# Optimization experiments

Hardware: AMD Instinct MI355X
Metric: run time of the kernel (lower is better)

## Reference

```python
import jax, jax.numpy as jnp
import numpy as np

N_NODES = 50000
N_EDGES = 800000
IN_CH = 256
HID_CH = 128


def setup_inputs() -> dict:
    key = jax.random.key(0)
    k1, k2, k3, k4, k5 = jax.random.split(key, 5)
    x = jax.random.normal(k1, (N_NODES, IN_CH), dtype=jnp.float32)
    edge_index = jax.random.randint(k2, (2, N_EDGES), 0, N_NODES, dtype=jnp.int64)
    edge_weight = jax.random.uniform(k3, (N_EDGES,), dtype=jnp.float32)
    W = jax.random.normal(k4, (IN_CH, HID_CH), dtype=jnp.float32) * (1.0 / np.sqrt(IN_CH))
    b = jnp.zeros((HID_CH,), dtype=jnp.float32)
    alpha = jnp.full((HID_CH,), 0.25, dtype=jnp.float32)  # PReLU default init
    return {"x": x, "edge_index": edge_index, "edge_weight": edge_weight,
            "W": W, "b": b, "alpha": alpha}


def reference(x, edge_index, edge_weight, W, b, alpha):
    """GCNConv (with self-loops + symmetric normalization) followed by PReLU."""
    N = x.shape[0]
    row, col = edge_index[0], edge_index[1]
    # add self-loops with weight 1 (PyG gcn_norm default, add_self_loops=True)
    loop = jnp.arange(N, dtype=row.dtype)
    row = jnp.concatenate([row, loop])
    col = jnp.concatenate([col, loop])
    ew = jnp.concatenate([edge_weight, jnp.ones((N,), dtype=edge_weight.dtype)])
    # degree from edge weights, scattered at destination (col)
    deg = jax.ops.segment_sum(ew, col, num_segments=N)
    deg_inv_sqrt = jnp.where(deg > 0, jax.lax.rsqrt(deg), 0.0)
    norm = deg_inv_sqrt[row] * ew * deg_inv_sqrt[col]  # [E+N]
    # linear transform then gather-scale-scatter aggregation
    h = x @ W                               # [N, HID]
    msg = h[row] * norm[:, None]            # [E+N, HID]
    out = jax.ops.segment_sum(msg, col, num_segments=N) + b
    # PReLU with per-channel slope
    return jnp.where(out >= 0, out, alpha * out)
```

## Files before the change

kernel.cpp:

```cpp
#include <hip/hip_runtime.h>

#define NN 50000
#define NE 800000
#define KD 256
#define CD 128
#define NB 196
#define GEMM_BLOCKS 782
#define HIST_BLOCKS 3125

typedef __attribute__((ext_vector_type(8))) short short8;
typedef __attribute__((ext_vector_type(4))) float floatx4;

__device__ inline unsigned short f2bf(float f) {
    unsigned u = __float_as_uint(f);
    unsigned r = (u + 0x7FFFu + ((u >> 16) & 1u)) >> 16;
    return (unsigned short)r;
}
__device__ inline float bf2f_lo(unsigned u) { return __uint_as_float(u << 16); }
__device__ inline float bf2f_hi(unsigned u) { return __uint_as_float(u & 0xFFFF0000u); }

__global__ __launch_bounds__(256) void fused_gemm_hist(
        const float* __restrict__ x, const unsigned short* __restrict__ Wt,
        unsigned short* __restrict__ hb,
        const int* __restrict__ col, const float* __restrict__ ew,
        unsigned long long* __restrict__ packed, unsigned short* __restrict__ rank) {
    __shared__ unsigned short As[64][40];
    __shared__ unsigned short Bs[128][40];

    if (blockIdx.x >= GEMM_BLOCKS) {
        int e = (blockIdx.x - GEMM_BLOCKS) * 256 + threadIdx.x;
        if (e < NE) {
            unsigned long long p = (1ull << 40)
                                 + (unsigned long long)(ew[e] * 4294967296.0f);
            unsigned long long old = atomicAdd(&packed[col[e]], p);
            rank[e] = (unsigned short)(old >> 40);
        }
        return;
    }

    const int tid  = threadIdx.x;
    const int wave = tid >> 6;
    const int lane = tid & 63;
    const int row0 = blockIdx.x * 64;
    const int m0   = wave * 16;
    const int lr   = lane & 15;
    const int quad = lane >> 4;

    const int ar = tid >> 2;
    const int aq = tid & 3;
    const int bn = tid >> 1;
    const int bh = (tid & 1) * 16;

    floatx4 acc[8];
#pragma unroll
    for (int nt = 0; nt < 8; nt++) acc[nt] = (floatx4){0.f, 0.f, 0.f, 0.f};

    for (int kt = 0; kt < 8; kt++) {
        const int k0 = kt * 32;
        union { short8 v; unsigned short u[8]; } av;
        const int gr = row0 + ar;
        if (gr < NN) {
            const float* xp = x + (size_t)gr * KD + k0 + aq * 8;
            float4 f0 = *(const float4*)xp;
            float4 f1 = *(const float4*)(xp + 4);
            av.u[0] = f2bf(f0.x); av.u[1] = f2bf(f0.y);
            av.u[2] = f2bf(f0.z); av.u[3] = f2bf(f0.w);
            av.u[4] = f2bf(f1.x); av.u[5] = f2bf(f1.y);
            av.u[6] = f2bf(f1.z); av.u[7] = f2bf(f1.w);
        } else {
            av.v = (short8){0,0,0,0,0,0,0,0};
        }
        *(short8*)&As[ar][aq * 8] = av.v;
        const unsigned short* wp = Wt + (size_t)bn * KD + k0 + bh;
        *(short8*)&Bs[bn][bh]     = *(const short8*)wp;
        *(short8*)&Bs[bn][bh + 8] = *(const short8*)(wp + 8);
        __syncthreads();
        short8 af = *(const short8*)&As[m0 + lr][quad * 8];
#pragma unroll
        for (int nt = 0; nt < 8; nt++) {
            short8 bfr = *(const short8*)&Bs[nt * 16 + lr][quad * 8];
            acc[nt] = __builtin_amdgcn_mfma_f32_16x16x32_bf16(af, bfr, acc[nt], 0, 0, 0);
        }
        __syncthreads();
    }

#pragma unroll
    for (int i = 0; i < 4; i++) {
        const int grow = row0 + m0 + quad * 4 + i;
        if (grow < NN) {
            unsigned short* hp = hb + (size_t)grow * CD + lr;
#pragma unroll
            for (int nt = 0; nt < 8; nt++)
                hp[nt * 16] = f2bf(acc[nt][i]);
        }
    }
}

__global__ __launch_bounds__(256) void scan_blocks(const unsigned long long* __restrict__ packed,
                                                   int* __restrict__ local,
                                                   int* __restrict__ partials) {
    __shared__ int sm[256];
    const int t = threadIdx.x;
    const int g = blockIdx.x * 256 + t;
    int v = (g < NN) ? (int)(packed[g] >> 40) : 0;
    sm[t] = v;
    __syncthreads();
#pragma unroll
    for (int off = 1; off < 256; off <<= 1) {
        int u = (t >= off) ? sm[t - off] : 0;
        __syncthreads();
        sm[t] += u;
        __syncthreads();
    }
    local[g] = sm[t] - v;
    if (t == 255) partials[blockIdx.x] = sm[t];
}

__global__ __launch_bounds__(256) void scan_apply(const int* __restrict__ local,
                                                  const int* __restrict__ partials,
                                                  const unsigned long long* __restrict__ packed,
                                                  int* __restrict__ start,
                                                  float* __restrict__ dinv) {
    __shared__ int sm[256];
    const int t = threadIdx.x;
    const int b = blockIdx.x;
    sm[t] = (t < b) ? partials[t] : 0;
    __syncthreads();
#pragma unroll
    for (int off = 128; off > 0; off >>= 1) {
        if (t < off) sm[t] += sm[t + off];
        __syncthreads();
    }
    const int base = sm[0];
    const int g = b * 256 + t;
    if (g < NN) {
        start[g] = local[g] + base;
        float degs = (float)(packed[g] & ((1ull << 40) - 1)) * (1.0f / 4294967296.0f);
        dinv[g] = rsqrtf(1.0f + degs);
    }
    if (g == 0) start[NN] = NE;
}

__global__ __launch_bounds__(256) void meta_write(const int* __restrict__ row,
                                                  const int* __restrict__ col,
                                                  const float* __restrict__ ew,
                                                  const unsigned short* __restrict__ rank,
                                                  const int* __restrict__ start,
                                                  const float* __restrict__ dinv,
                                                  int2* __restrict__ meta) {
    int e = blockIdx.x * 256 + threadIdx.x;
    if (e >= NE) return;
    int c = col[e];
    int r = row[e];
    int pos = start[c] + rank[e];
    float f = dinv[r] * ew[e];
    meta[pos] = make_int2(r, __float_as_int(f));
}

__global__ __launch_bounds__(256) void w_transpose(const float* __restrict__ W,
                                                   unsigned short* __restrict__ Wt) {
    __shared__ unsigned short t[32][33];
    const int bk = blockIdx.x * 32;
    const int bn = blockIdx.y * 32;
    const int tx = threadIdx.x & 31;
    const int ty = threadIdx.x >> 5;
#pragma unroll
    for (int i = 0; i < 32; i += 8)
        t[ty + i][tx] = f2bf(W[(size_t)(bk + ty + i) * CD + bn + tx]);
    __syncthreads();
#pragma unroll
    for (int i = 0; i < 32; i += 8)
        Wt[(size_t)(bn + ty + i) * KD + bk + tx] = t[tx][ty + i];
}

__global__ __launch_bounds__(256) void aggregate(const int* __restrict__ start,
                                                 const int2* __restrict__ meta,
                                                 const unsigned short* __restrict__ hb,
                                                 const float* __restrict__ dinv,
                                                 const float* __restrict__ bias,
                                                 const float* __restrict__ alpha,
                                                 float* __restrict__ out) {
    int n = blockIdx.x * 4 + (threadIdx.x >> 6);
    if (n >= NN) return;
    n = __builtin_amdgcn_readfirstlane(n);
    const int lane = threadIdx.x & 63;
    const int s = __builtin_amdgcn_readfirstlane(start[n]);
    const int e = __builtin_amdgcn_readfirstlane(start[n + 1]);

    float A0[8], A1[8];
#pragma unroll
    for (int j = 0; j < 8; j++) { A0[j] = 0.f; A1[j] = 0.f; }

    int i = s;
    for (; i + 8 <= e; i += 8) {
        int2 m[8];
        unsigned u[8];
#pragma unroll
        for (int j = 0; j < 8; j++) m[j] = meta[i + j];
#pragma unroll
        for (int j = 0; j < 8; j++)
            u[j] = *(const unsigned*)(hb + (size_t)m[j].x * CD + lane * 2);
#pragma unroll
        for (int j = 0; j < 8; j++) {
            float w = __int_as_float(m[j].y);
            A0[j] = fmaf(w, bf2f_lo(u[j]), A0[j]);
            A1[j] = fmaf(w, bf2f_hi(u[j]), A1[j]);
        }
    }
    for (; i < e; i++) {
        int2 m = meta[i];
        unsigned u = *(const unsigned*)(hb + (size_t)m.x * CD + lane * 2);
        float w = __int_as_float(m.y);
        A0[0] = fmaf(w, bf2f_lo(u), A0[0]);
        A1[0] = fmaf(w, bf2f_hi(u), A1[0]);
    }
#pragma unroll
    for (int j = 1; j < 8; j++) { A0[0] += A0[j]; A1[0] += A1[j]; }

    const float dc = dinv[n];
    unsigned us = *(const unsigned*)(hb + (size_t)n * CD + lane * 2);
    const int ch = lane * 2;
    float o0 = dc * A0[0] + dc * dc * bf2f_lo(us) + bias[ch];
    float o1 = dc * A1[0] + dc * dc * bf2f_hi(us) + bias[ch + 1];
    o0 = o0 >= 0.f ? o0 : alpha[ch] * o0;
    o1 = o1 >= 0.f ? o1 : alpha[ch + 1] * o1;
    *(float2*)(out + (size_t)n * CD + ch) = make_float2(o0, o1);
}

extern "C" void kernel_launch(void* const* d_in, const int* in_sizes, int n_in,
                              void* d_out, int out_size, void* d_ws, size_t ws_size,
                              hipStream_t stream) {
    const float* x     = (const float*)d_in[0];
    const int*   eidx  = (const int*)d_in[1];
    const float* ew    = (const float*)d_in[2];
    const float* Wm    = (const float*)d_in[3];
    const float* bias  = (const float*)d_in[4];
    const float* alpha = (const float*)d_in[5];
    const int* row = eidx;
    const int* col = eidx + NE;

    float* out = (float*)d_out;

    char* ws = (char*)d_ws;
    unsigned long long* packed = (unsigned long long*)(ws);
    int*   start    = (int*)(ws + 400000);
    int*   local    = (int*)(ws + 600016);
    int*   partials = (int*)(ws + 800720);
    float* dinv     = (float*)(ws + 801504);
    unsigned short* rank = (unsigned short*)(ws + 1001504);
    int2*  meta     = (int2*)(ws + 2601504);
    unsigned short* Wt = (unsigned short*)(ws + 9001504);
    unsigned short* hb = (unsigned short*)(ws + 9067040);

    hipMemsetAsync(ws, 0, 400000, stream);
    w_transpose   <<<dim3(8, 4), 256, 0, stream>>>(Wm, Wt);
    fused_gemm_hist<<<GEMM_BLOCKS + HIST_BLOCKS, 256, 0, stream>>>(
                        x, Wt, hb, col, ew, packed, rank);
    scan_blocks   <<<NB, 256, 0, stream>>>(packed, local, partials);
    scan_apply    <<<NB, 256, 0, stream>>>(local, partials, packed, start, dinv);
    meta_write    <<<(NE + 255) / 256, 256, 0, stream>>>(row, col, ew, rank, start, dinv, meta);
    aggregate     <<<(NN + 3) / 4, 256, 0, stream>>>(start, meta, hb, dinv, bias, alpha, out);
}
```

Measured before the change: 205.5 us.

## Replicate degree histogram four ways and pack edge metadata into 32 bits

The edge histogram now spreads its atomics over four replicated counter arrays, selected by block index, to cut atomic contention. The scan kernels sum the four copies, and per-copy base offsets are emitted so meta_write can place each edge. Edge metadata shrinks from int2 to one 32-bit word holding a 16-bit row index and a bf16 weight, halving metadata traffic in aggregate. The cost is a larger memset plus extra reads in the scans. Precision is lower, and the packing assumes row indices fit in 16 bits, which fails for 50000 nodes (above 65535 is fine, but 50000 < 65536 holds).

```diff
diff --git a/kernel.cpp b/kernel.cpp
--- a/kernel.cpp
+++ b/kernel.cpp
@@ -23,13 +23,15 @@
         const float* __restrict__ x, const unsigned short* __restrict__ Wt,
         unsigned short* __restrict__ hb,
         const int* __restrict__ col, const float* __restrict__ ew,
-        unsigned long long* __restrict__ packed, unsigned short* __restrict__ rank) {
+        unsigned long long* __restrict__ packedAll, unsigned short* __restrict__ rank) {
     __shared__ unsigned short As[64][40];
     __shared__ unsigned short Bs[128][40];
 
     if (blockIdx.x >= GEMM_BLOCKS) {
-        int e = (blockIdx.x - GEMM_BLOCKS) * 256 + threadIdx.x;
+        const int hblk = blockIdx.x - GEMM_BLOCKS;
+        int e = hblk * 256 + threadIdx.x;
         if (e < NE) {
+            unsigned long long* packed = packedAll + (size_t)(hblk & 3) * NN;
             unsigned long long p = (1ull << 40)
                                  + (unsigned long long)(ew[e] * 4294967296.0f);
             unsigned long long old = atomicAdd(&packed[col[e]], p);
@@ -96,13 +98,18 @@
     }
 }
 
-__global__ __launch_bounds__(256) void scan_blocks(const unsigned long long* __restrict__ packed,
+__global__ __launch_bounds__(256) void scan_blocks(const unsigned long long* __restrict__ packedAll,
                                                    int* __restrict__ local,
                                                    int* __restrict__ partials) {
     __shared__ int sm[256];
     const int t = threadIdx.x;
     const int g = blockIdx.x * 256 + t;
-    int v = (g < NN) ? (int)(packed[g] >> 40) : 0;
+    int v = 0;
+    if (g < NN) {
+#pragma unroll
+        for (int c = 0; c < 4; c++)
+            v += (int)(packedAll[(size_t)c * NN + g] >> 40);
+    }
     sm[t] = v;
     __syncthreads();
 #pragma unroll
@@ -118,8 +125,9 @@
 
 __global__ __launch_bounds__(256) void scan_apply(const int* __restrict__ local,
                                                   const int* __restrict__ partials,
-                                                  const unsigned long long* __restrict__ packed,
+                                                  const unsigned long long* __restrict__ packedAll,
                                                   int* __restrict__ start,
+                                                  int4* __restrict__ base4,
                                                   float* __restrict__ dinv) {
     __shared__ int sm[256];
     const int t = threadIdx.x;
@@ -134,8 +142,18 @@
     const int base = sm[0];
     const int g = b * 256 + t;
     if (g < NN) {
-        start[g] = local[g] + base;
-        float degs = (float)(packed[g] & ((1ull << 40) - 1)) * (1.0f / 4294967296.0f);
+        int cc[4];
+        unsigned long long lowsum = 0;
+#pragma unroll
+        for (int c = 0; c < 4; c++) {
+            unsigned long long p = packedAll[(size_t)c * NN + g];
+            cc[c] = (int)(p >> 40);
+            lowsum += p & ((1ull << 40) - 1);
+        }
+        const int s = local[g] + base;
+        start[g] = s;
+        base4[g] = make_int4(s, s + cc[0], s + cc[0] + cc[1], s + cc[0] + cc[1] + cc[2]);
+        float degs = (float)lowsum * (1.0f / 4294967296.0f);
         dinv[g] = rsqrtf(1.0f + degs);
     }
     if (g == 0) start[NN] = NE;
@@ -145,16 +163,19 @@
                                                   const int* __restrict__ col,
                                                   const float* __restrict__ ew,
                                                   const unsigned short* __restrict__ rank,
-                                                  const int* __restrict__ start,
+                                                  const int4* __restrict__ base4,
                                                   const float* __restrict__ dinv,
-                                                  int2* __restrict__ meta) {
+                                                  unsigned* __restrict__ meta) {
     int e = blockIdx.x * 256 + threadIdx.x;
     if (e >= NE) return;
+    const int copy = blockIdx.x & 3;
     int c = col[e];
     int r = row[e];
-    int pos = start[c] + rank[e];
-    float f = dinv[r] * ew[e];
-    meta[pos] = make_int2(r, __float_as_int(f));
+    int4 b4 = base4[c];
+    int base = (copy == 0) ? b4.x : (copy == 1) ? b4.y : (copy == 2) ? b4.z : b4.w;
+    int pos = base + rank[e];
+    unsigned short wbf = f2bf(dinv[r] * ew[e]);
+    meta[pos] = ((unsigned)wbf << 16) | (unsigned)r;
 }
 
 __global__ __launch_bounds__(256) void w_transpose(const float* __restrict__ W,
@@ -174,7 +195,7 @@
 }
 
 __global__ __launch_bounds__(256) void aggregate(const int* __restrict__ start,
-                                                 const int2* __restrict__ meta,
+                                                 const unsigned* __restrict__ meta,
                                                  const unsigned short* __restrict__ hb,
                                                  const float* __restrict__ dinv,
                                                  const float* __restrict__ bias,
@@ -193,24 +214,23 @@
 
     int i = s;
     for (; i + 8 <= e; i += 8) {
-        int2 m[8];
-        unsigned u[8];
+        unsigned m[8], u[8];
 #pragma unroll
         for (int j = 0; j < 8; j++) m[j] = meta[i + j];
 #pragma unroll
         for (int j = 0; j < 8; j++)
-            u[j] = *(const unsigned*)(hb + (size_t)m[j].x * CD + lane * 2);
+            u[j] = *(const unsigned*)(hb + (size_t)(m[j] & 0xFFFFu) * CD + lane * 2);
 #pragma unroll
         for (int j = 0; j < 8; j++) {
-            float w = __int_as_float(m[j].y);
+            float w = __uint_as_float(m[j] & 0xFFFF0000u);
             A0[j] = fmaf(w, bf2f_lo(u[j]), A0[j]);
             A1[j] = fmaf(w, bf2f_hi(u[j]), A1[j]);
         }
     }
     for (; i < e; i++) {
-        int2 m = meta[i];
-        unsigned u = *(const unsigned*)(hb + (size_t)m.x * CD + lane * 2);
-        float w = __int_as_float(m.y);
+        unsigned m = meta[i];
+        unsigned u = *(const unsigned*)(hb + (size_t)(m & 0xFFFFu) * CD + lane * 2);
+        float w = __uint_as_float(m & 0xFFFF0000u);
         A0[0] = fmaf(w, bf2f_lo(u), A0[0]);
         A1[0] = fmaf(w, bf2f_hi(u), A1[0]);
     }
@@ -242,22 +262,23 @@
     float* out = (float*)d_out;
 
     char* ws = (char*)d_ws;
-    unsigned long long* packed = (unsigned long long*)(ws);
-    int*   start    = (int*)(ws + 400000);
-    int*   local    = (int*)(ws + 600016);
-    int*   partials = (int*)(ws + 800720);
-    float* dinv     = (float*)(ws + 801504);
-    unsigned short* rank = (unsigned short*)(ws + 1001504);
-    int2*  meta     = (int2*)(ws + 2601504);
-    unsigned short* Wt = (unsigned short*)(ws + 9001504);
-    unsigned short* hb = (unsigned short*)(ws + 9067040);
-
-    hipMemsetAsync(ws, 0, 400000, stream);
+    unsigned long long* packedAll = (unsigned long long*)(ws);
+    int*   start    = (int*)(ws + 1600000);
+    int*   local    = (int*)(ws + 1800016);
+    int*   partials = (int*)(ws + 2000720);
+    float* dinv     = (float*)(ws + 2001504);
+    unsigned short* rank = (unsigned short*)(ws + 2201504);
+    int4*  base4    = (int4*)(ws + 3801504);
+    unsigned* meta  = (unsigned*)(ws + 4601504);
+    unsigned short* Wt = (unsigned short*)(ws + 7801504);
+    unsigned short* hb = (unsigned short*)(ws + 7867040);
+
+    hipMemsetAsync(ws, 0, 1600000, stream);
     w_transpose   <<<dim3(8, 4), 256, 0, stream>>>(Wm, Wt);
     fused_gemm_hist<<<GEMM_BLOCKS + HIST_BLOCKS, 256, 0, stream>>>(
-                        x, Wt, hb, col, ew, packed, rank);
-    scan_blocks   <<<NB, 256, 0, stream>>>(packed, local, partials);
-    scan_apply    <<<NB, 256, 0, stream>>>(local, partials, packed, start, dinv);
-    meta_write    <<<(NE + 255) / 256, 256, 0, stream>>>(row, col, ew, rank, start, dinv, meta);
+                        x, Wt, hb, col, ew, packedAll, rank);
+    scan_blocks   <<<NB, 256, 0, stream>>>(packedAll, local, partials);
+    scan_apply    <<<NB, 256, 0, stream>>>(local, partials, packedAll, start, base4, dinv);
+    meta_write    <<<(NE + 255) / 256, 256, 0, stream>>>(row, col, ew, rank, base4, dinv, meta);
     aggregate     <<<(NN + 3) / 4, 256, 0, stream>>>(start, meta, hb, dinv, bias, alpha, out);
 }
```

Result: no change. 203.3 us (-1.1%).

## Fuse all stages into one cooperative persistent kernel with grid syncs and packed meta

Applied to the files above, without the earlier changes.

Replaces the memset and six separate kernel launches with a single cooperative kernel of 1024 persistent blocks. Stages are separated by grid.sync, and edge loops become grid-strided. The edge metadata is packed into 32 bits, a 16-bit row index plus a bf16 weight, which halves meta traffic in the aggregation but lowers weight precision. This targets launch gaps and inter-kernel idle time, at the cost of grid-wide barriers, fewer blocks doing the histogram atomics, and a 4-blocks-per-CU occupancy constraint.

```diff
diff --git a/kernel.cpp b/kernel.cpp
--- a/kernel.cpp
+++ b/kernel.cpp
@@ -1,4 +1,7 @@
 #include <hip/hip_runtime.h>
+#include <hip/hip_cooperative_groups.h>
+
+namespace cg = cooperative_groups;
 
 #define NN 50000
 #define NE 800000
@@ -6,7 +9,8 @@
 #define CD 128
 #define NB 196
 #define GEMM_BLOCKS 782
-#define HIST_BLOCKS 3125
+#define GRID 1024
+#define HIST_BLOCKS (GRID - GEMM_BLOCKS)
 
 typedef __attribute__((ext_vector_type(8))) short short8;
 typedef __attribute__((ext_vector_type(4))) float floatx4;
@@ -19,212 +23,195 @@
 __device__ inline float bf2f_lo(unsigned u) { return __uint_as_float(u << 16); }
 __device__ inline float bf2f_hi(unsigned u) { return __uint_as_float(u & 0xFFFF0000u); }
 
-__global__ __launch_bounds__(256) void fused_gemm_hist(
-        const float* __restrict__ x, const unsigned short* __restrict__ Wt,
-        unsigned short* __restrict__ hb,
+__global__ __launch_bounds__(256, 4) void mega(
+        const float* __restrict__ x, const float* __restrict__ Wm,
         const int* __restrict__ col, const float* __restrict__ ew,
-        unsigned long long* __restrict__ packed, unsigned short* __restrict__ rank) {
+        const int* __restrict__ row,
+        const float* __restrict__ bias, const float* __restrict__ alpha,
+        float* __restrict__ out,
+        unsigned long long* __restrict__ packed,
+        int* __restrict__ start, int* __restrict__ local,
+        int* __restrict__ partials, float* __restrict__ dinv,
+        unsigned short* __restrict__ rank, unsigned* __restrict__ meta,
+        unsigned short* __restrict__ Wt, unsigned short* __restrict__ hb) {
+    cg::grid_group grid = cg::this_grid();
     __shared__ unsigned short As[64][40];
     __shared__ unsigned short Bs[128][40];
 
-    if (blockIdx.x >= GEMM_BLOCKS) {
-        int e = (blockIdx.x - GEMM_BLOCKS) * 256 + threadIdx.x;
-        if (e < NE) {
+    const int tid = threadIdx.x;
+    const int b   = blockIdx.x;
+
+    if (b < 32) {
+        unsigned short (*t)[33] = (unsigned short (*)[33])&As[0][0];
+        const int bk = (b >> 2) * 32;
+        const int bn = (b & 3) * 32;
+        const int tx = tid & 31;
+        const int ty = tid >> 5;
+#pragma unroll
+        for (int i = 0; i < 32; i += 8)
+            t[ty + i][tx] = f2bf(Wm[(size_t)(bk + ty + i) * CD + bn + tx]);
+        __syncthreads();
+#pragma unroll
+        for (int i = 0; i < 32; i += 8)
+            Wt[(size_t)(bn + ty + i) * KD + bk + tx] = t[tx][ty + i];
+    } else {
+        int idx = (b - 32) * 256 + tid;
+        if (idx < NN) packed[idx] = 0;
+    }
+    grid.sync();
+
+    if (b < GEMM_BLOCKS) {
+        const int wave = tid >> 6;
+        const int lane = tid & 63;
+        const int row0 = b * 64;
+        const int m0   = wave * 16;
+        const int lr   = lane & 15;
+        const int quad = lane >> 4;
+        const int ar = tid >> 2;
+        const int aq = tid & 3;
+        const int bn = tid >> 1;
+        const int bh = (tid & 1) * 16;
+
+        floatx4 acc[8];
+#pragma unroll
+        for (int nt = 0; nt < 8; nt++) acc[nt] = (floatx4){0.f, 0.f, 0.f, 0.f};
+
+        for (int kt = 0; kt < 8; kt++) {
+            const int k0 = kt * 32;
+            union { short8 v; unsigned short u[8]; } av;
+            const int gr = row0 + ar;
+            if (gr < NN) {
+                const float* xp = x + (size_t)gr * KD + k0 + aq * 8;
+                float4 f0 = *(const float4*)xp;
+                float4 f1 = *(const float4*)(xp + 4);
+                av.u[0] = f2bf(f0.x); av.u[1] = f2bf(f0.y);
+                av.u[2] = f2bf(f0.z); av.u[3] = f2bf(f0.w);
+                av.u[4] = f2bf(f1.x); av.u[5] = f2bf(f1.y);
+                av.u[6] = f2bf(f1.z); av.u[7] = f2bf(f1.w);
+            } else {
+                av.v = (short8){0,0,0,0,0,0,0,0};
+            }
+            __syncthreads();
+            *(short8*)&As[ar][aq * 8] = av.v;
+            const unsigned short* wp = Wt + (size_t)bn * KD + k0 + bh;
+            *(short8*)&Bs[bn][bh]     = *(const short8*)wp;
+            *(short8*)&Bs[bn][bh + 8] = *(const short8*)(wp + 8);
+            __syncthreads();
+            short8 af = *(const short8*)&As[m0 + lr][quad * 8];
+#pragma unroll
+            for (int nt = 0; nt < 8; nt++) {
+                short8 bfr = *(const short8*)&Bs[nt * 16 + lr][quad * 8];
+                acc[nt] = __builtin_amdgcn_mfma_f32_16x16x32_bf16(af, bfr, acc[nt], 0, 0, 0);
+            }
+        }
+#pragma unroll
+        for (int i = 0; i < 4; i++) {
+            const int grow = row0 + m0 + quad * 4 + i;
+            if (grow < NN) {
+                unsigned short* hp = hb + (size_t)grow * CD + lr;
+#pragma unroll
+                for (int nt = 0; nt < 8; nt++)
+                    hp[nt * 16] = f2bf(acc[nt][i]);
+            }
+        }
+    } else {
+        for (int e = (b - GEMM_BLOCKS) * 256 + tid; e < NE; e += HIST_BLOCKS * 256) {
             unsigned long long p = (1ull << 40)
                                  + (unsigned long long)(ew[e] * 4294967296.0f);
             unsigned long long old = atomicAdd(&packed[col[e]], p);
             rank[e] = (unsigned short)(old >> 40);
         }
-        return;
-    }
-
-    const int tid  = threadIdx.x;
-    const int wave = tid >> 6;
+    }
+    grid.sync();
+
+    int* sm = (int*)&As[0][0];
+    if (b < NB) {
+        const int g = b * 256 + tid;
+        int v = (g < NN) ? (int)(packed[g] >> 40) : 0;
+        sm[tid] = v;
+        __syncthreads();
+#pragma unroll
+        for (int off = 1; off < 256; off <<= 1) {
+            int u = (tid >= off) ? sm[tid - off] : 0;
+            __syncthreads();
+            sm[tid] += u;
+            __syncthreads();
+        }
+        local[g] = sm[tid] - v;
+        if (tid == 255) partials[b] = sm[tid];
+    }
+    grid.sync();
+
+    if (b < NB) {
+        sm[tid] = (tid < b) ? partials[tid] : 0;
+        __syncthreads();
+#pragma unroll
+        for (int off = 128; off > 0; off >>= 1) {
+            if (tid < off) sm[tid] += sm[tid + off];
+            __syncthreads();
+        }
+        const int base = sm[0];
+        const int g = b * 256 + tid;
+        if (g < NN) {
+            start[g] = local[g] + base;
+            float degs = (float)(packed[g] & ((1ull << 40) - 1)) * (1.0f / 4294967296.0f);
+            dinv[g] = rsqrtf(1.0f + degs);
+        }
+        if (g == 0) start[NN] = NE;
+    }
+    grid.sync();
+
+    for (int e = b * 256 + tid; e < NE; e += GRID * 256) {
+        int c = col[e];
+        int r = row[e];
+        int pos = start[c] + rank[e];
+        unsigned short wbf = f2bf(dinv[r] * ew[e]);
+        meta[pos] = ((unsigned)wbf << 16) | (unsigned)r;
+    }
+    grid.sync();
+
     const int lane = tid & 63;
-    const int row0 = blockIdx.x * 64;
-    const int m0   = wave * 16;
-    const int lr   = lane & 15;
-    const int quad = lane >> 4;
-
-    const int ar = tid >> 2;
-    const int aq = tid & 3;
-    const int bn = tid >> 1;
-    const int bh = (tid & 1) * 16;
-
-    floatx4 acc[8];
-#pragma unroll
-    for (int nt = 0; nt < 8; nt++) acc[nt] = (floatx4){0.f, 0.f, 0.f, 0.f};
-
-    for (int kt = 0; kt < 8; kt++) {
-        const int k0 = kt * 32;
-        union { short8 v; unsigned short u[8]; } av;
-        const int gr = row0 + ar;
-        if (gr < NN) {
-            const float* xp = x + (size_t)gr * KD + k0 + aq * 8;
-            float4 f0 = *(const float4*)xp;
-            float4 f1 = *(const float4*)(xp + 4);
-            av.u[0] = f2bf(f0.x); av.u[1] = f2bf(f0.y);
-            av.u[2] = f2bf(f0.z); av.u[3] = f2bf(f0.w);
-            av.u[4] = f2bf(f1.x); av.u[5] = f2bf(f1.y);
-            av.u[6] = f2bf(f1.z); av.u[7] = f2bf(f1.w);
-        } else {
-            av.v = (short8){0,0,0,0,0,0,0,0};
-        }
-        *(short8*)&As[ar][aq * 8] = av.v;
-        const unsigned short* wp = Wt + (size_t)bn * KD + k0 + bh;
-        *(short8*)&Bs[bn][bh]     = *(const short8*)wp;
-        *(short8*)&Bs[bn][bh + 8] = *(const short8*)(wp + 8);
-        __syncthreads();
-        short8 af = *(const short8*)&As[m0 + lr][quad * 8];
-#pragma unroll
-        for (int nt = 0; nt < 8; nt++) {
-            short8 bfr = *(const short8*)&Bs[nt * 16 + lr][quad * 8];
-            acc[nt] = __builtin_amdgcn_mfma_f32_16x16x32_bf16(af, bfr, acc[nt], 0, 0, 0);
-        }
-        __syncthreads();
-    }
-
-#pragma unroll
-    for (int i = 0; i < 4; i++) {
-        const int grow = row0 + m0 + quad * 4 + i;
-        if (grow < NN) {
-            unsigned short* hp = hb + (size_t)grow * CD + lr;
-#pragma unroll
-            for (int nt = 0; nt < 8; nt++)
-                hp[nt * 16] = f2bf(acc[nt][i]);
-        }
-    }
-}
-
-__global__ __launch_bounds__(256) void scan_blocks(const unsigned long long* __restrict__ packed,
-                                                   int* __restrict__ local,
-                                                   int* __restrict__ partials) {
-    __shared__ int sm[256];
-    const int t = threadIdx.x;
-    const int g = blockIdx.x * 256 + t;
-    int v = (g < NN) ? (int)(packed[g] >> 40) : 0;
-    sm[t] = v;
-    __syncthreads();
-#pragma unroll
-    for (int off = 1; off < 256; off <<= 1) {
-        int u = (t >= off) ? sm[t - off] : 0;
-        __syncthreads();
-        sm[t] += u;
-        __syncthreads();
-    }
-    local[g] = sm[t] - v;
-    if (t == 255) partials[blockIdx.x] = sm[t];
-}
-
-__global__ __launch_bounds__(256) void scan_apply(const int* __restrict__ local,
-                                                  const int* __restrict__ partials,
-                                                  const unsigned long long* __restrict__ packed,
-                                                  int* __restrict__ start,
-                                                  float* __restrict__ dinv) {
-    __shared__ int sm[256];
-    const int t = threadIdx.x;
-    const int b = blockIdx.x;
-    sm[t] = (t < b) ? partials[t] : 0;
-    __syncthreads();
-#pragma unroll
-    for (int off = 128; off > 0; off >>= 1) {
-        if (t < off) sm[t] += sm[t + off];
-        __syncthreads();
-    }
-    const int base = sm[0];
-    const int g = b * 256 + t;
-    if (g < NN) {
-        start[g] = local[g] + base;
-        float degs = (float)(packed[g] & ((1ull << 40) - 1)) * (1.0f / 4294967296.0f);
-        dinv[g] = rsqrtf(1.0f + degs);
-    }
-    if (g == 0) start[NN] = NE;
-}
-
-__global__ __launch_bounds__(256) void meta_write(const int* __restrict__ row,
-                                                  const int* __restrict__ col,
-                                                  const float* __restrict__ ew,
-                                                  const unsigned short* __restrict__ rank,
-                                                  const int* __restrict__ start,
-                                                  const float* __restrict__ dinv,
-                                                  int2* __restrict__ meta) {
-    int e = blockIdx.x * 256 + threadIdx.x;
-    if (e >= NE) return;
-    int c = col[e];
-    int r = row[e];
-    int pos = start[c] + rank[e];
-    float f = dinv[r] * ew[e];
-    meta[pos] = make_int2(r, __float_as_int(f));
-}
-
-__global__ __launch_bounds__(256) void w_transpose(const float* __restrict__ W,
-                                                   unsigned short* __restrict__ Wt) {
-    __shared__ unsigned short t[32][33];
-    const int bk = blockIdx.x * 32;
-    const int bn = blockIdx.y * 32;
-    const int tx = threadIdx.x & 31;
-    const int ty = threadIdx.x >> 5;
-#pragma unroll
-    for (int i = 0; i < 32; i += 8)
-        t[ty + i][tx] = f2bf(W[(size_t)(bk + ty + i) * CD + bn + tx]);
-    __syncthreads();
-#pragma unroll
-    for (int i = 0; i < 32; i += 8)
-        Wt[(size_t)(bn + ty + i) * KD + bk + tx] = t[tx][ty + i];
-}
-
-__global__ __launch_bounds__(256) void aggregate(const int* __restrict__ start,
-                                                 const int2* __restrict__ meta,
-                                                 const unsigned short* __restrict__ hb,
-                                                 const float* __restrict__ dinv,
-                                                 const float* __restrict__ bias,
-                                                 const float* __restrict__ alpha,
-                                                 float* __restrict__ out) {
-    int n = blockIdx.x * 4 + (threadIdx.x >> 6);
-    if (n >= NN) return;
-    n = __builtin_amdgcn_readfirstlane(n);
-    const int lane = threadIdx.x & 63;
-    const int s = __builtin_amdgcn_readfirstlane(start[n]);
-    const int e = __builtin_amdgcn_readfirstlane(start[n + 1]);
-
-    float A0[8], A1[8];
-#pragma unroll
-    for (int j = 0; j < 8; j++) { A0[j] = 0.f; A1[j] = 0.f; }
-
-    int i = s;
-    for (; i + 8 <= e; i += 8) {
-        int2 m[8];
-        unsigned u[8];
-#pragma unroll
-        for (int j = 0; j < 8; j++) m[j] = meta[i + j];
-#pragma unroll
-        for (int j = 0; j < 8; j++)
-            u[j] = *(const unsigned*)(hb + (size_t)m[j].x * CD + lane * 2);
-#pragma unroll
-        for (int j = 0; j < 8; j++) {
-            float w = __int_as_float(m[j].y);
-            A0[j] = fmaf(w, bf2f_lo(u[j]), A0[j]);
-            A1[j] = fmaf(w, bf2f_hi(u[j]), A1[j]);
-        }
-    }
-    for (; i < e; i++) {
-        int2 m = meta[i];
-        unsigned u = *(const unsigned*)(hb + (size_t)m.x * CD + lane * 2);
-        float w = __int_as_float(m.y);
-        A0[0] = fmaf(w, bf2f_lo(u), A0[0]);
-        A1[0] = fmaf(w, bf2f_hi(u), A1[0]);
-    }
-#pragma unroll
-    for (int j = 1; j < 8; j++) { A0[0] += A0[j]; A1[0] += A1[j]; }
-
-    const float dc = dinv[n];
-    unsigned us = *(const unsigned*)(hb + (size_t)n * CD + lane * 2);
-    const int ch = lane * 2;
-    float o0 = dc * A0[0] + dc * dc * bf2f_lo(us) + bias[ch];
-    float o1 = dc * A1[0] + dc * dc * bf2f_hi(us) + bias[ch + 1];
-    o0 = o0 >= 0.f ? o0 : alpha[ch] * o0;
-    o1 = o1 >= 0.f ? o1 : alpha[ch + 1] * o1;
-    *(float2*)(out + (size_t)n * CD + ch) = make_float2(o0, o1);
+    const int wv   = b * 4 + (tid >> 6);
+    for (int n = wv; n < NN; n += GRID * 4) {
+        const int s = __builtin_amdgcn_readfirstlane(start[n]);
+        const int e = __builtin_amdgcn_readfirstlane(start[n + 1]);
+        float A0[8], A1[8];
+#pragma unroll
+        for (int j = 0; j < 8; j++) { A0[j] = 0.f; A1[j] = 0.f; }
+        int i = s;
+        for (; i + 8 <= e; i += 8) {
+            unsigned m[8], u[8];
+#pragma unroll
+            for (int j = 0; j < 8; j++) m[j] = meta[i + j];
+#pragma unroll
+            for (int j = 0; j < 8; j++)
+                u[j] = *(const unsigned*)(hb + (size_t)(m[j] & 0xFFFFu) * CD + lane * 2);
+#pragma unroll
+            for (int j = 0; j < 8; j++) {
+                float w = __uint_as_float(m[j] & 0xFFFF0000u);
+                A0[j] = fmaf(w, bf2f_lo(u[j]), A0[j]);
+                A1[j] = fmaf(w, bf2f_hi(u[j]), A1[j]);
+            }
+        }
+        for (; i < e; i++) {
+            unsigned m = meta[i];
+            unsigned u = *(const unsigned*)(hb + (size_t)(m & 0xFFFFu) * CD + lane * 2);
+            float w = __uint_as_float(m & 0xFFFF0000u);
+            A0[0] = fmaf(w, bf2f_lo(u), A0[0]);
+            A1[0] = fmaf(w, bf2f_hi(u), A1[0]);
+        }
+#pragma unroll
+        for (int j = 1; j < 8; j++) { A0[0] += A0[j]; A1[0] += A1[j]; }
+
+        const float dc = dinv[n];
+        unsigned us = *(const unsigned*)(hb + (size_t)n * CD + lane * 2);
+        const int ch = lane * 2;
+        float o0 = dc * A0[0] + dc * dc * bf2f_lo(us) + bias[ch];
+        float o1 = dc * A1[0] + dc * dc * bf2f_hi(us) + bias[ch + 1];
+        o0 = o0 >= 0.f ? o0 : alpha[ch] * o0;
+        o1 = o1 >= 0.f ? o1 : alpha[ch + 1] * o1;
+        *(float2*)(out + (size_t)n * CD + ch) = make_float2(o0, o1);
+    }
 }
 
 extern "C" void kernel_launch(void* const* d_in, const int* in_sizes, int n_in,
@@ -248,16 +235,16 @@
     int*   partials = (int*)(ws + 800720);
     float* dinv     = (float*)(ws + 801504);
     unsigned short* rank = (unsigned short*)(ws + 1001504);
-    int2*  meta     = (int2*)(ws + 2601504);
-    unsigned short* Wt = (unsigned short*)(ws + 9001504);
-    unsigned short* hb = (unsigned short*)(ws + 9067040);
-
-    hipMemsetAsync(ws, 0, 400000, stream);
-    w_transpose   <<<dim3(8, 4), 256, 0, stream>>>(Wm, Wt);
-    fused_gemm_hist<<<GEMM_BLOCKS + HIST_BLOCKS, 256, 0, stream>>>(
-                        x, Wt, hb, col, ew, packed, rank);
-    scan_blocks   <<<NB, 256, 0, stream>>>(packed, local, partials);
-    scan_apply    <<<NB, 256, 0, stream>>>(local, partials, packed, start, dinv);
-    meta_write    <<<(NE + 255) / 256, 256, 0, stream>>>(row, col, ew, rank, start, dinv, meta);
-    aggregate     <<<(NN + 3) / 4, 256, 0, stream>>>(start, meta, hb, dinv, bias, alpha, out);
+    unsigned* meta  = (unsigned*)(ws + 2601504);
+    unsigned short* Wt = (unsigned short*)(ws + 5801504);
+    unsigned short* hb = (unsigned short*)(ws + 5867040);
+
+    void* args[] = {
+        (void*)&x, (void*)&Wm, (void*)&col, (void*)&ew, (void*)&row,
+        (void*)&bias, (void*)&alpha, (void*)&out,
+        (void*)&packed, (void*)&start, (void*)&local, (void*)&partials,
+        (void*)&dinv, (void*)&rank, (void*)&meta, (void*)&Wt, (void*)&hb
+    };
+    hipLaunchCooperativeKernel((const void*)mega, dim3(GRID), dim3(256),
+                               args, 0, stream);
 }
```

Result: slower. 814.7 us (+296.4%).

## Fuse prep and scan/meta kernels cooperatively and pack edge metadata into 32 bits

Applied to the files above, without the earlier changes.

Merges the memset and W transpose into one prep kernel. The two scan kernels and the meta-write kernel become a single cooperative kernel that uses grid-wide syncs, which cuts launch count and inter-kernel gaps. Per-edge metadata shrinks from int2 to one 32-bit word: a 16-bit source index plus a bf16 weight. This halves the metadata traffic read in aggregation. The cost is lower precision in the edge weights, a dependency on the node count fitting in 16 bits, and grid.sync overhead.

```diff
diff --git a/kernel.cpp b/kernel.cpp
--- a/kernel.cpp
+++ b/kernel.cpp
@@ -1,4 +1,7 @@
 #include <hip/hip_runtime.h>
+#include <hip/hip_cooperative_groups.h>
+
+namespace cg = cooperative_groups;
 
 #define NN 50000
 #define NE 800000
@@ -7,6 +10,7 @@
 #define NB 196
 #define GEMM_BLOCKS 782
 #define HIST_BLOCKS 3125
+#define MIDG 256
 
 typedef __attribute__((ext_vector_type(8))) short short8;
 typedef __attribute__((ext_vector_type(4))) float floatx4;
@@ -18,6 +22,28 @@
 }
 __device__ inline float bf2f_lo(unsigned u) { return __uint_as_float(u << 16); }
 __device__ inline float bf2f_hi(unsigned u) { return __uint_as_float(u & 0xFFFF0000u); }
+
+__global__ __launch_bounds__(256) void prep(const float* __restrict__ Wm,
+                                            unsigned short* __restrict__ Wt,
+                                            unsigned long long* __restrict__ packed) {
+    if (blockIdx.x < 32) {
+        __shared__ unsigned short t[32][33];
+        const int bk = (blockIdx.x >> 2) * 32;
+        const int bn = (blockIdx.x & 3) * 32;
+        const int tx = threadIdx.x & 31;
+        const int ty = threadIdx.x >> 5;
+#pragma unroll
+        for (int i = 0; i < 32; i += 8)
+            t[ty + i][tx] = f2bf(Wm[(size_t)(bk + ty + i) * CD + bn + tx]);
+        __syncthreads();
+#pragma unroll
+        for (int i = 0; i < 32; i += 8)
+            Wt[(size_t)(bn + ty + i) * KD + bk + tx] = t[tx][ty + i];
+    } else {
+        int idx = (blockIdx.x - 32) * 256 + threadIdx.x;
+        if (idx < NN) packed[idx] = 0;
+    }
+}
 
 __global__ __launch_bounds__(256) void fused_gemm_hist(
         const float* __restrict__ x, const unsigned short* __restrict__ Wt,
@@ -96,85 +122,65 @@
     }
 }
 
-__global__ __launch_bounds__(256) void scan_blocks(const unsigned long long* __restrict__ packed,
-                                                   int* __restrict__ local,
-                                                   int* __restrict__ partials) {
-    __shared__ int sm[256];
-    const int t = threadIdx.x;
-    const int g = blockIdx.x * 256 + t;
-    int v = (g < NN) ? (int)(packed[g] >> 40) : 0;
-    sm[t] = v;
-    __syncthreads();
-#pragma unroll
-    for (int off = 1; off < 256; off <<= 1) {
-        int u = (t >= off) ? sm[t - off] : 0;
-        __syncthreads();
-        sm[t] += u;
-        __syncthreads();
-    }
-    local[g] = sm[t] - v;
-    if (t == 255) partials[blockIdx.x] = sm[t];
-}
-
-__global__ __launch_bounds__(256) void scan_apply(const int* __restrict__ local,
-                                                  const int* __restrict__ partials,
-                                                  const unsigned long long* __restrict__ packed,
-                                                  int* __restrict__ start,
-                                                  float* __restrict__ dinv) {
+__global__ __launch_bounds__(256) void mid(
+        const unsigned long long* __restrict__ packed,
+        int* __restrict__ local, int* __restrict__ partials,
+        int* __restrict__ start, float* __restrict__ dinv,
+        const int* __restrict__ row, const int* __restrict__ col,
+        const float* __restrict__ ew, const unsigned short* __restrict__ rank,
+        unsigned* __restrict__ meta) {
+    cg::grid_group grid = cg::this_grid();
     __shared__ int sm[256];
     const int t = threadIdx.x;
     const int b = blockIdx.x;
-    sm[t] = (t < b) ? partials[t] : 0;
-    __syncthreads();
-#pragma unroll
-    for (int off = 128; off > 0; off >>= 1) {
-        if (t < off) sm[t] += sm[t + off];
-        __syncthreads();
-    }
-    const int base = sm[0];
-    const int g = b * 256 + t;
-    if (g < NN) {
-        start[g] = local[g] + base;
-        float degs = (float)(packed[g] & ((1ull << 40) - 1)) * (1.0f / 4294967296.0f);
-        dinv[g] = rsqrtf(1.0f + degs);
-    }
-    if (g == 0) start[NN] = NE;
-}
-
-__global__ __launch_bounds__(256) void meta_write(const int* __restrict__ row,
-                                                  const int* __restrict__ col,
-                                                  const float* __restrict__ ew,
-                                                  const unsigned short* __restrict__ rank,
-                                                  const int* __restrict__ start,
-                                                  const float* __restrict__ dinv,
-                                                  int2* __restrict__ meta) {
-    int e = blockIdx.x * 256 + threadIdx.x;
-    if (e >= NE) return;
-    int c = col[e];
-    int r = row[e];
-    int pos = start[c] + rank[e];
-    float f = dinv[r] * ew[e];
-    meta[pos] = make_int2(r, __float_as_int(f));
-}
-
-__global__ __launch_bounds__(256) void w_transpose(const float* __restrict__ W,
-                                                   unsigned short* __restrict__ Wt) {
-    __shared__ unsigned short t[32][33];
-    const int bk = blockIdx.x * 32;
-    const int bn = blockIdx.y * 32;
-    const int tx = threadIdx.x & 31;
-    const int ty = threadIdx.x >> 5;
-#pragma unroll
-    for (int i = 0; i < 32; i += 8)
-        t[ty + i][tx] = f2bf(W[(size_t)(bk + ty + i) * CD + bn + tx]);
-    __syncthreads();
-#pragma unroll
-    for (int i = 0; i < 32; i += 8)
-        Wt[(size_t)(bn + ty + i) * KD + bk + tx] = t[tx][ty + i];
+
+    if (b < NB) {
+        const int g = b * 256 + t;
+        int v = (g < NN) ? (int)(packed[g] >> 40) : 0;
+        sm[t] = v;
+        __syncthreads();
+#pragma unroll
+        for (int off = 1; off < 256; off <<= 1) {
+            int u = (t >= off) ? sm[t - off] : 0;
+            __syncthreads();
+            sm[t] += u;
+            __syncthreads();
+        }
+        local[g] = sm[t] - v;
+        if (t == 255) partials[b] = sm[t];
+    }
+    grid.sync();
+
+    if (b < NB) {
+        sm[t] = (t < b) ? partials[t] : 0;
+        __syncthreads();
+#pragma unroll
+        for (int off = 128; off > 0; off >>= 1) {
+            if (t < off) sm[t] += sm[t + off];
+            __syncthreads();
+        }
+        const int base = sm[0];
+        const int g = b * 256 + t;
+        if (g < NN) {
+            start[g] = local[g] + base;
+            float degs = (float)(packed[g] & ((1ull << 40) - 1)) * (1.0f / 4294967296.0f);
+            dinv[g] = rsqrtf(1.0f + degs);
+        }
+        if (g == 0) start[NN] = NE;
+    }
+    grid.sync();
+
+    for (int e = b * 256 + t; e < NE; e += MIDG * 256) {
+        int c = col[e];
+        int r = row[e];
+        int pos = start[c] + rank[e];
+        unsigned short wbf = f2bf(dinv[r] * ew[e]);
+        meta[pos] = ((unsigned)wbf << 16) | (unsigned)r;
+    }
 }
 
 __global__ __launch_bounds__(256) void aggregate(const int* __restrict__ start,
-                                                 const int2* __restrict__ meta,
+                                                 const unsigned* __restrict__ meta,
                                                  const unsigned short* __restrict__ hb,
                                                  const float* __restrict__ dinv,
                                                  const float* __restrict__ bias,
@@ -193,24 +199,23 @@
 
     int i = s;
     for (; i + 8 <= e; i += 8) {
-        int2 m[8];
-        unsigned u[8];
+        unsigned m[8], u[8];
 #pragma unroll
         for (int j = 0; j < 8; j++) m[j] = meta[i + j];
 #pragma unroll
         for (int j = 0; j < 8; j++)
-            u[j] = *(const unsigned*)(hb + (size_t)m[j].x * CD + lane * 2);
+            u[j] = *(const unsigned*)(hb + (size_t)(m[j] & 0xFFFFu) * CD + lane * 2);
 #pragma unroll
         for (int j = 0; j < 8; j++) {
-            float w = __int_as_float(m[j].y);
+            float w = __uint_as_float(m[j] & 0xFFFF0000u);
             A0[j] = fmaf(w, bf2f_lo(u[j]), A0[j]);
             A1[j] = fmaf(w, bf2f_hi(u[j]), A1[j]);
         }
     }
     for (; i < e; i++) {
-        int2 m = meta[i];
-        unsigned u = *(const unsigned*)(hb + (size_t)m.x * CD + lane * 2);
-        float w = __int_as_float(m.y);
+        unsigned m = meta[i];
+        unsigned u = *(const unsigned*)(hb + (size_t)(m & 0xFFFFu) * CD + lane * 2);
+        float w = __uint_as_float(m & 0xFFFF0000u);
         A0[0] = fmaf(w, bf2f_lo(u), A0[0]);
         A1[0] = fmaf(w, bf2f_hi(u), A1[0]);
     }
@@ -248,16 +253,21 @@
     int*   partials = (int*)(ws + 800720);
     float* dinv     = (float*)(ws + 801504);
     unsigned short* rank = (unsigned short*)(ws + 1001504);
-    int2*  meta     = (int2*)(ws + 2601504);
-    unsigned short* Wt = (unsigned short*)(ws + 9001504);
-    unsigned short* hb = (unsigned short*)(ws + 9067040);
-
-    hipMemsetAsync(ws, 0, 400000, stream);
-    w_transpose   <<<dim3(8, 4), 256, 0, stream>>>(Wm, Wt);
+    unsigned* meta  = (unsigned*)(ws + 2601504);
+    unsigned short* Wt = (unsigned short*)(ws + 5801504);
+    unsigned short* hb = (unsigned short*)(ws + 5867040);
+
+    prep          <<<228, 256, 0, stream>>>(Wm, Wt, packed);
     fused_gemm_hist<<<GEMM_BLOCKS + HIST_BLOCKS, 256, 0, stream>>>(
                         x, Wt, hb, col, ew, packed, rank);
-    scan_blocks   <<<NB, 256, 0, stream>>>(packed, local, partials);
-    scan_apply    <<<NB, 256, 0, stream>>>(local, partials, packed, start, dinv);
-    meta_write    <<<(NE + 255) / 256, 256, 0, stream>>>(row, col, ew, rank, start, dinv, meta);
+
+    void* margs[] = {
+        (void*)&packed, (void*)&local, (void*)&partials, (void*)&start,
+        (void*)&dinv, (void*)&row, (void*)&col, (void*)&ew,
+        (void*)&rank, (void*)&meta
+    };
+    hipLaunchCooperativeKernel((const void*)mid, dim3(MIDG), dim3(256),
+                               margs, 0, stream);
+
     aggregate     <<<(NN + 3) / 4, 256, 0, stream>>>(start, meta, hb, dinv, bias, alpha, out);
 }
```

New measurement: 272.6 us. 1.33x slower.
